# Optimization experiments

Hardware: AMD Instinct MI355X
Metric: run time of the kernel (lower is better)

## Reference

```python
import jax, jax.numpy as jnp
import numpy as np

B, V, C_IN, C_OUT = 4, 8, 32, 32
H, W = 256, 256
G = H * W
K_NEIGHBORS = 3


def compute_adjacency_tilde(extrinsics, k):
    Bv, Vv = extrinsics.shape[:2]
    R = extrinsics[:, :, :3, :3]
    t = extrinsics[:, :, :3, 3]
    # camera centers: -R^T t
    centers = -jnp.einsum('bvji,bvj->bvi', R, t)                 # (B,V,3)
    diff = centers[:, :, None, :] - centers[:, None, :, :]
    dist_sq = jnp.sum(diff * diff, axis=-1)                      # (B,V,V)
    eye = jnp.eye(Vv, dtype=bool)
    sim = jnp.where(eye, -jnp.inf, -dist_sq)
    A_overlap = 1.0 / (1.0 + jnp.sqrt(dist_sq + 1e-6))
    if 0 < k < Vv:
        _, topk_idx = jax.lax.top_k(sim, k)                      # (B,V,k)
        mask = jnp.sum(jax.nn.one_hot(topk_idx, Vv, dtype=jnp.float32), axis=-2) > 0
        A = A_overlap * mask.astype(A_overlap.dtype)
    else:
        A = A_overlap
    A = jnp.where(eye, 1.0, A)                                   # diagonal = 1
    deg = jnp.sum(A, axis=-1, keepdims=True)
    A_tilde = A / (deg + (deg == 0).astype(deg.dtype))
    return A, A_tilde


def setup_inputs() -> dict:
    key = jax.random.key(0)
    k1, k2, k3, k4, k5 = jax.random.split(key, 5)
    features = jax.random.normal(k1, (B, V, G, C_IN), dtype=jnp.float32)
    # projected pixel coords in [0, W-1] x [0, H-1]
    uv = jax.random.uniform(k2, (B, V, V, G, 2), dtype=jnp.float32)
    xy_coords = uv * jnp.array([W - 1, H - 1], dtype=jnp.float32)
    extrinsics = jax.random.normal(k3, (B, V, 4, 4), dtype=jnp.float32)
    W_lin = jax.random.normal(k4, (C_IN, C_OUT), dtype=jnp.float32) * 0.1
    b_lin = jax.random.normal(k5, (C_OUT,), dtype=jnp.float32) * 0.01
    return {"features": features, "xy_coords": xy_coords, "extrinsics": extrinsics,
            "W_lin": W_lin, "b_lin": b_lin}


def reference(features, xy_coords, extrinsics, W_lin, b_lin):
    feats = features @ W_lin + b_lin                              # (B,V,G,D)
    Bv, Vv, Gv, D = feats.shape
    HW = H * W
    A, A_tilde = compute_adjacency_tilde(extrinsics, K_NEIGHBORS)
    # flattened pixel indices per (batch, src view, tgt view, gaussian)
    x = jnp.clip(jnp.round(xy_coords[..., 0]), 0, W - 1).astype(jnp.int32)
    y = jnp.clip(jnp.round(xy_coords[..., 1]), 0, H - 1).astype(jnp.int32)
    idx = y * W + x                                               # (B,Vsrc,Vtgt,G)
    batch_off = jnp.arange(Bv, dtype=jnp.int32)[:, None] * HW
    outs = []
    for i in range(Vv):  # small fixed number of target views
        w_i = A_tilde[:, i][:, :, None, None]                     # (B,Vsrc,1,1)
        data = (feats * w_i).reshape(Bv * Vv * Gv, D)
        seg = (idx[:, :, i].reshape(Bv, Vv * Gv) + batch_off).reshape(-1)
        grid = jax.ops.segment_sum(data, seg, num_segments=Bv * HW)
        grid = grid.reshape(Bv, HW, D)                            # (B,HW,D)
        self_idx = idx[:, i, i]                                   # (B,G)
        outs.append(jnp.take_along_axis(grid, self_idx[..., None], axis=1))
    stacked = jnp.stack(outs, axis=1)                             # (B,V,G,D)
    return stacked, A
```

## Files before the change

### kernel.cpp

```cpp
#include <hip/hip_runtime.h>
#include <math.h>

#define NB 4
#define NV 8
#define NC 32
#define NG 65536
#define IMGW 256
#define NBI 32
#define RSPLIT 8
#define RBINS (NG / RSPLIT)
#define K4SPLIT 32
#define K4BINS (NG / K4SPLIT)
#define K4CAP 24576
#define CAP4A 1272
#define PART_STRIDE 19456
#define START_STRIDE 65544
#define SORT_STRIDE (1u << 20)
#define SENTINEL (8u << 27)

static constexpr long long STACKED_ELEMS = (long long)NB * NV * NG * NC;

typedef __attribute__((ext_vector_type(8))) short short8;
typedef __attribute__((ext_vector_type(4))) float f32x4;
typedef __attribute__((ext_vector_type(4))) unsigned int u32x4;
typedef __attribute__((ext_vector_type(4))) float f32x4c;

static constexpr size_t OFF_AT    = 0;
static constexpr size_t OFF_RTOT  = 1024;
static constexpr size_t OFF_RBASE = 2048;
static constexpr size_t OFF_GSC   = 3584;
static constexpr size_t OFF_START = 8192;
static constexpr size_t OFF_CNT   = OFF_START + (size_t)NBI * START_STRIDE * 4;
static constexpr size_t OFF_PIX   = OFF_CNT + (size_t)NBI * NG * 4;
static constexpr size_t OFF_SORT  = OFF_PIX + (size_t)NBI * NV * NG * 2;
static constexpr size_t OFF_FB16  = OFF_SORT + (size_t)NBI * SORT_STRIDE * 4;
static constexpr size_t OFF_PARTS = OFF_FB16;

__device__ __forceinline__ unsigned short f2bf(float f)
{
    unsigned int u = __float_as_uint(f);
    return (unsigned short)((u + 0x7FFFu + ((u >> 16) & 1u)) >> 16);
}

__global__ __launch_bounds__(256) void adj_kernel(const float* __restrict__ ext,
                                                  float* __restrict__ A_out,
                                                  float* __restrict__ At_out)
{
    __shared__ float ctr[NB * NV][3];
    __shared__ float Dsh[NB * NV * NV];
    int t = threadIdx.x;
    if (t < NB * NV) {
        const float* E = ext + t * 16;
        #pragma unroll
        for (int i = 0; i < 3; i++) {
            float s = E[0 * 4 + i] * E[0 * 4 + 3]
                    + E[1 * 4 + i] * E[1 * 4 + 3]
                    + E[2 * 4 + i] * E[2 * 4 + 3];
            ctr[t][i] = -s;
        }
    }
    __syncthreads();
    {
        int b = t >> 6, i = (t >> 3) & 7, j = t & 7;
        float dx = ctr[b * 8 + i][0] - ctr[b * 8 + j][0];
        float dy = ctr[b * 8 + i][1] - ctr[b * 8 + j][1];
        float dz = ctr[b * 8 + i][2] - ctr[b * 8 + j][2];
        Dsh[t] = dx * dx + dy * dy + dz * dz;
    }
    __syncthreads();
    if (t < NB * NV) {
        int ri = t & 7;
        const float* drow = &Dsh[t * 8];
        bool chosen[8] = {false, false, false, false, false, false, false, false};
        for (int n = 0; n < 3; n++) {
            int best = -1; float bs = -3.0e38f;
            for (int j2 = 0; j2 < 8; j2++) {
                if (j2 == ri || chosen[j2]) continue;
                float s = -drow[j2];
                if (s > bs) { bs = s; best = j2; }
            }
            chosen[best] = true;
        }
        float row[8]; float deg = 0.f;
        #pragma unroll
        for (int j2 = 0; j2 < 8; j2++) {
            float a = 0.f;
            if (j2 == ri)        a = 1.0f;
            else if (chosen[j2]) a = 1.0f / (1.0f + sqrtf(drow[j2] + 1e-6f));
            row[j2] = a; deg += a;
        }
        float dn = deg + (deg == 0.f ? 1.f : 0.f);
        #pragma unroll
        for (int j2 = 0; j2 < 8; j2++) {
            A_out[t * 8 + j2]  = row[j2];
            At_out[t * 8 + j2] = row[j2] / dn;
        }
    }
}

__global__ __launch_bounds__(256) void k1_pix(const float2* __restrict__ xy,
                                              unsigned short* __restrict__ pixarr)
{
    unsigned int base = blockIdx.x * 1024 + threadIdx.x;
    #pragma unroll
    for (int k = 0; k < 4; k++) {
        unsigned int tid = base + k * 256;
        float2 p = xy[tid];
        float px = fminf(fmaxf(rintf(p.x), 0.f), (float)(IMGW - 1));
        float py = fminf(fmaxf(rintf(p.y), 0.f), (float)(IMGW - 1));
        unsigned int pix = (unsigned int)py * IMGW + (unsigned int)px;
        unsigned int g = tid & 0xFFFFu;
        unsigned int i = (tid >> 16) & 7u;
        unsigned int j = (tid >> 19) & 7u;
        unsigned int b = tid >> 22;
        unsigned int bi = (b << 3) | i;
        pixarr[(((bi << 3) | j) << 16) | g] = (unsigned short)pix;
    }
}

__global__ __launch_bounds__(1024) void k2_hist(const unsigned short* __restrict__ pixarr,
                                                unsigned int* __restrict__ cnt,
                                                unsigned int* __restrict__ rtot)
{
    __shared__ unsigned int hist[RBINS];
    int t = threadIdx.x;
    unsigned int bi = blockIdx.x & 31u;
    unsigned int r  = blockIdx.x >> 5;
    unsigned int r0 = r * RBINS;
    for (int k = t; k < RBINS; k += 1024) hist[k] = 0;
    __syncthreads();
    const uint4* src = (const uint4*)(pixarr + ((size_t)bi << 19));
    for (int it = 0; it < 16; it++) {
        uint4 vv[4];
        #pragma unroll
        for (int q = 0; q < 4; q++)
            vv[q] = src[t + (it * 4 + q) * 1024];
        #pragma unroll
        for (int q = 0; q < 4; q++) {
            const unsigned int* vw = (const unsigned int*)&vv[q];
            #pragma unroll
            for (int h = 0; h < 4; h++) {
                unsigned int w = vw[h];
                unsigned int p0 = (w & 0xFFFFu) - r0;
                unsigned int p1 = (w >> 16) - r0;
                if (p0 < RBINS) atomicAdd(&hist[p0], 1u);
                if (p1 < RBINS) atomicAdd(&hist[p1], 1u);
            }
        }
    }
    __syncthreads();
    unsigned int* dst = cnt + ((size_t)bi << 16) + r0;
    unsigned int psum = 0;
    for (int k = t; k < RBINS; k += 1024) {
        unsigned int v = hist[k];
        dst[k] = v;
        psum += (v + 7u) & ~7u;
    }
    __syncthreads();
    hist[t] = psum;
    __syncthreads();
    for (int off = 512; off; off >>= 1) {
        if (t < off) hist[t] += hist[t + off];
        __syncthreads();
    }
    if (t == 0) rtot[bi * 8 + r] = hist[0];
}

__global__ __launch_bounds__(64) void k3b_rscan(const unsigned int* __restrict__ rtot,
                                                unsigned int* __restrict__ rbase)
{
    int t = threadIdx.x;
    if (t < 32) {
        unsigned int run = 0;
        #pragma unroll
        for (int q = 0; q < 8; q++) {
            rbase[t * 9 + q] = run;
            run += rtot[t * 8 + q];
        }
        rbase[t * 9 + 8] = run;
    }
}

__global__ __launch_bounds__(1024) void k3c_scan(const unsigned int* __restrict__ cnt,
                                                 const unsigned int* __restrict__ rbase,
                                                 unsigned int* __restrict__ start)
{
    __shared__ unsigned int lc[RBINS];
    __shared__ unsigned int bs[1024];
    int t = threadIdx.x;
    unsigned int bi = blockIdx.x & 31u;
    unsigned int r  = blockIdx.x >> 5;
    unsigned int r0 = r * RBINS;
    const unsigned int* c = cnt + ((size_t)bi << 16) + r0;
    #pragma unroll
    for (int q = 0; q < 8; q++)
        lc[q * 1024 + t] = (c[q * 1024 + t] + 7u) & ~7u;
    __syncthreads();
    unsigned int v[8]; unsigned int s = 0;
    #pragma unroll
    for (int k = 0; k < 8; k++) { v[k] = s; s += lc[t * 8 + k]; }
    bs[t] = s;
    __syncthreads();
    for (int off = 1; off < 1024; off <<= 1) {
        unsigned int u = (t >= off) ? bs[t - off] : 0u;
        __syncthreads();
        bs[t] += u;
        __syncthreads();
    }
    unsigned int base = rbase[bi * 9 + r] + bs[t] - s;
    #pragma unroll
    for (int k = 0; k < 8; k++) lc[t * 8 + k] = base + v[k];
    __syncthreads();
    unsigned int* st_ = start + (size_t)bi * START_STRIDE + r0;
    #pragma unroll
    for (int q = 0; q < 8; q++)
        st_[q * 1024 + t] = lc[q * 1024 + t];
    if (r == 7 && t == 0)
        start[(size_t)bi * START_STRIDE + NG] = rbase[bi * 9 + 8];
}

__global__ __launch_bounds__(1024) void k4a_part(const unsigned short* __restrict__ pixarr,
                                                 unsigned int* __restrict__ gsc,
                                                 unsigned int* __restrict__ parts)
{
    extern __shared__ unsigned int dynA[];
    unsigned int* cur32 = dynA;
    unsigned int* res   = dynA + 32;
    unsigned int* lcnt  = dynA + 64;
    unsigned int* lbuck = dynA + 96;
    int t = threadIdx.x;
    unsigned int bi    = blockIdx.x & 31u;
    unsigned int chunk = blockIdx.x >> 5;
    if (t < 32) cur32[t] = 0;
    __syncthreads();
    const uint4* src = (const uint4*)(pixarr + ((size_t)bi << 19)) + (chunk << 12);
    unsigned int idx0 = chunk << 15;
    #pragma unroll
    for (int it = 0; it < 4; it++) {
        uint4 v = src[t + it * 1024];
        unsigned int base_idx = idx0 + (t + it * 1024) * 8;
        const unsigned int* vw = (const unsigned int*)&v;
        #pragma unroll
        for (int h = 0; h < 8; h++) {
            unsigned int pix = (h & 1) ? (vw[h >> 1] >> 16) : (vw[h >> 1] & 0xFFFFu);
            unsigned int sub = pix >> 11;
            unsigned int pv = ((pix & 0x7FFu) << 19) | (base_idx + h);
            unsigned int slot = atomicAdd(&cur32[sub], 1u);
            if (slot < CAP4A) {
                lbuck[sub * CAP4A + slot] = pv;
            } else {
                unsigned int gs = atomicAdd(&gsc[(bi << 5) | sub], 1u);
                parts[(size_t)((bi << 5) | sub) * PART_STRIDE + gs] = pv;
            }
        }
    }
    __syncthreads();
    if (t < 32) {
        unsigned int n = cur32[t];
        n = n < CAP4A ? n : CAP4A;
        lcnt[t] = n;
        res[t] = atomicAdd(&gsc[(bi << 5) | t], n);
    }
    __syncthreads();
    for (int s = 0; s < 32; s++) {
        unsigned int n = lcnt[s];
        unsigned int b0 = res[s];
        unsigned int* dst = parts + (size_t)((bi << 5) | s) * PART_STRIDE + b0;
        const unsigned int* sb = lbuck + s * CAP4A;
        for (unsigned int k = t; k < n; k += 1024) dst[k] = sb[k];
    }
}

__global__ __launch_bounds__(1024) void k4b_fill(const unsigned int* __restrict__ gsc,
                                                 const unsigned int* __restrict__ parts,
                                                 const unsigned int* __restrict__ start,
                                                 unsigned int* __restrict__ sorted)
{
    extern __shared__ unsigned int dynB[];
    unsigned int* cur = dynB;
    unsigned int* buf = dynB + K4BINS;
    int t = threadIdx.x;
    unsigned int bi  = blockIdx.x & 31u;
    unsigned int sub = blockIdx.x >> 5;
    unsigned int bin0 = sub * K4BINS;
    const unsigned int* stg = start + (size_t)bi * START_STRIDE;
    unsigned int base = stg[bin0];
    unsigned int end  = stg[bin0 + K4BINS];
    unsigned int size = end - base;
    unsigned int n = gsc[(bi << 5) | sub];
    const unsigned int* seg = parts + (size_t)((bi << 5) | sub) * PART_STRIDE;
    unsigned int* dstbase = sorted + (size_t)bi * SORT_STRIDE;

    if (size <= K4CAP) {
        #pragma unroll 2
        for (int k = t; k < K4BINS; k += 1024) cur[k] = stg[bin0 + k] - base;
        for (int k = t; k < (int)size; k += 1024) buf[k] = SENTINEL;
        __syncthreads();
        for (unsigned int k = t; k < n; k += 1024) {
            unsigned int pv = seg[k];
            unsigned int bin = pv >> 19;
            unsigned int slot = atomicAdd(&cur[bin], 1u);
            buf[slot] = (((pv >> 16) & 7u) << 27) | ((pv & 0x7FFFFu) << 6);
        }
        __syncthreads();
        uint4* gdst = (uint4*)(dstbase + base);
        const uint4* lsrc = (const uint4*)buf;
        int n4 = (int)(size >> 2);
        for (int k = t; k < n4; k += 1024) gdst[k] = lsrc[k];
    } else {
        #pragma unroll 2
        for (int k = t; k < K4BINS; k += 1024) cur[k] = stg[bin0 + k];
        __syncthreads();
        for (unsigned int k = t; k < n; k += 1024) {
            unsigned int pv = seg[k];
            unsigned int bin = pv >> 19;
            unsigned int slot = atomicAdd(&cur[bin], 1u);
            dstbase[slot] = (((pv >> 16) & 7u) << 27) | ((pv & 0x7FFFFu) << 6);
        }
        __syncthreads();
        for (int k = t; k < K4BINS; k += 1024) {
            unsigned int e = stg[bin0 + k + 1];
            for (unsigned int x = cur[k]; x < e; x++) dstbase[x] = SENTINEL;
        }
    }
}

__global__ __launch_bounds__(256) void kf_conv(const float* __restrict__ src,
                                               ushort4* __restrict__ dst)
{
    unsigned int base = blockIdx.x * 1024 + threadIdx.x;
    #pragma unroll
    for (int k = 0; k < 4; k++) {
        unsigned int idx = base + k * 256;
        f32x4c v = __builtin_nontemporal_load((const f32x4c*)(src) + idx);
        ushort4 o;
        o.x = f2bf(v.x); o.y = f2bf(v.y); o.z = f2bf(v.z); o.w = f2bf(v.w);
        dst[idx] = o;
    }
}

__global__ __launch_bounds__(256, 4) void b_gather(
    const unsigned short* __restrict__ fb16,
    const unsigned short* __restrict__ pixarr,
    const unsigned int* __restrict__ start,
    const unsigned int* __restrict__ sorted,
    const float* __restrict__ Wlin,
    const float* __restrict__ blin,
    const float* __restrict__ At,
    float* __restrict__ out,
    int b)
{
    __shared__ float At9[NBI][16];
    int t = threadIdx.x;
    int c4 = t & 7;
    int grp = t >> 3;

    unsigned int bidx = blockIdx.x;
    unsigned int i  = bidx & 7u;
    unsigned int gc = bidx >> 3;
    unsigned int bi = ((unsigned int)b << 3) | i;
    unsigned int g0 = gc << 5;
    unsigned int g = g0 + grp;
    unsigned int pix = pixarr[(((bi << 3) | i) << 16) | g];

    At9[t >> 3][t & 7] = At[t];
    At9[t >> 3][8 + (t & 7)] = 0.f;

    int l = t & 63;
    short8 bf0, bf1;
    #pragma unroll
    for (int j = 0; j < 8; j++) {
        int kk = (l >> 4) * 8 + j;
        bf0[j] = (short)f2bf(Wlin[kk * NC + (l & 15)]);
        bf1[j] = (short)f2bf(Wlin[kk * NC + 16 + (l & 15)]);
    }

    const unsigned int* st = start + (size_t)bi * START_STRIDE;
    unsigned int s0 = st[pix];
    unsigned int e0 = st[pix + 1];
    const unsigned int* pl = sorted + (size_t)bi * SORT_STRIDE;
    const char* fbB = (const char*)fb16;
    unsigned int cb = c4 << 3;
    __syncthreads();

    const float* Atrow = At9[bi];
    float ax = 0.f, ay = 0.f, az = 0.f, aw = 0.f, wsum = 0.f;
    for (unsigned int k0 = s0; k0 < e0; k0 += 8) {
        u32x4 pa = __builtin_nontemporal_load((const u32x4*)(pl + k0));
        u32x4 pb = __builtin_nontemporal_load((const u32x4*)(pl + k0 + 4));
        unsigned int pv[8] = {pa.x, pa.y, pa.z, pa.w, pb.x, pb.y, pb.z, pb.w};
        uint2 uv[8];
        #pragma unroll
        for (int h = 0; h < 8; h++)
            uv[h] = *(const uint2*)(fbB + ((pv[h] & 0x01FFFFC0u) | cb));
        float wv[8];
        #pragma unroll
        for (int h = 0; h < 8; h++)
            wv[h] = Atrow[pv[h] >> 27];
        #pragma unroll
        for (int h = 0; h < 8; h++) {
            ax = fmaf(wv[h], __uint_as_float(uv[h].x << 16), ax);
            ay = fmaf(wv[h], __uint_as_float(uv[h].x & 0xFFFF0000u), ay);
            az = fmaf(wv[h], __uint_as_float(uv[h].y << 16), az);
            aw = fmaf(wv[h], __uint_as_float(uv[h].y & 0xFFFF0000u), aw);
            wsum += wv[h];
        }
    }

    int r = l & 15;
    int kb = l >> 4;
    int s0l = (((r & 7) << 3) | (kb << 1)) & 63;
    int s1l = s0l | 1;
    float v0x = __shfl(ax, s0l, 64), v0y = __shfl(ay, s0l, 64);
    float v0z = __shfl(az, s0l, 64), v0w = __shfl(aw, s0l, 64);
    float v1x = __shfl(ax, s1l, 64), v1y = __shfl(ay, s1l, 64);
    float v1z = __shfl(az, s1l, 64), v1w = __shfl(aw, s1l, 64);
    short8 af;
    if (r < 8) {
        af[0] = (short)f2bf(v0x); af[1] = (short)f2bf(v0y);
        af[2] = (short)f2bf(v0z); af[3] = (short)f2bf(v0w);
        af[4] = (short)f2bf(v1x); af[5] = (short)f2bf(v1y);
        af[6] = (short)f2bf(v1z); af[7] = (short)f2bf(v1w);
    } else {
        af = short8{0, 0, 0, 0, 0, 0, 0, 0};
    }
    float bias0 = blin[l & 15];
    float bias1 = blin[16 + (l & 15)];
    f32x4 c0, c1;
    #pragma unroll
    for (int q = 0; q < 4; q++) {
        int row = kb * 4 + q;
        float wvx = __shfl(wsum, (row << 3) & 63, 64);
        wvx = (row < 8) ? wvx : 0.f;
        c0[q] = bias0 * wvx;
        c1[q] = bias1 * wvx;
    }
    c0 = __builtin_amdgcn_mfma_f32_16x16x32_bf16(af, bf0, c0, 0, 0, 0);
    c1 = __builtin_amdgcn_mfma_f32_16x16x32_bf16(af, bf1, c1, 0, 0, 0);
    if (l < 32) {
        size_t rowbase = (((size_t)bi << 16) | g0) + (t >> 6) * 8;
        #pragma unroll
        for (int q = 0; q < 4; q++) {
            size_t rr = rowbase + (l >> 4) * 4 + q;
            __builtin_nontemporal_store(c0[q], &out[rr * NC + (l & 15)]);
            __builtin_nontemporal_store(c1[q], &out[rr * NC + 16 + (l & 15)]);
        }
    }
}

extern "C" void kernel_launch(void* const* d_in, const int* in_sizes, int n_in,
                              void* d_out, int out_size, void* d_ws, size_t ws_size,
                              hipStream_t stream)
{
    const float* features = (const float*)d_in[0];
    const float* xy       = (const float*)d_in[1];
    const float* ext      = (const float*)d_in[2];
    const float* Wlin     = (const float*)d_in[3];
    const float* blin     = (const float*)d_in[4];
    float* out = (float*)d_out;

    char* ws = (char*)d_ws;
    float*          At     = (float*)(ws + OFF_AT);
    unsigned int*   rtot   = (unsigned int*)(ws + OFF_RTOT);
    unsigned int*   rbase  = (unsigned int*)(ws + OFF_RBASE);
    unsigned int*   gsc    = (unsigned int*)(ws + OFF_GSC);
    unsigned int*   start  = (unsigned int*)(ws + OFF_START);
    unsigned int*   cnt    = (unsigned int*)(ws + OFF_CNT);
    unsigned short* pixarr = (unsigned short*)(ws + OFF_PIX);
    unsigned int*   sorted = (unsigned int*)(ws + OFF_SORT);
    unsigned int*   parts  = (unsigned int*)(ws + OFF_PARTS);
    unsigned short* fb16   = (unsigned short*)(ws + OFF_FB16);

    static const size_t k4a_lds = (96 + 32 * CAP4A) * sizeof(unsigned int);
    static const size_t k4b_lds = (K4BINS + K4CAP) * sizeof(unsigned int);
    hipFuncSetAttribute((const void*)k4a_part,
                        hipFuncAttributeMaxDynamicSharedMemorySize, (int)k4a_lds);
    hipFuncSetAttribute((const void*)k4b_fill,
                        hipFuncAttributeMaxDynamicSharedMemorySize, (int)k4b_lds);

    adj_kernel<<<1, 256, 0, stream>>>(ext, out + STACKED_ELEMS, At);

    k1_pix<<<(NB * NV * NV * NG) / 1024, 256, 0, stream>>>((const float2*)xy, pixarr);
    k2_hist<<<NBI * RSPLIT, 1024, 0, stream>>>(pixarr, cnt, rtot);
    k3b_rscan<<<1, 64, 0, stream>>>(rtot, rbase);
    k3c_scan<<<NBI * RSPLIT, 1024, 0, stream>>>(cnt, rbase, start);

    hipMemsetAsync(gsc, 0, 1024 * sizeof(unsigned int), stream);
    k4a_part<<<NBI * 16, 1024, k4a_lds, stream>>>(pixarr, gsc, parts);
    k4b_fill<<<NBI * K4SPLIT, 1024, k4b_lds, stream>>>(gsc, parts, start, sorted);

    for (int b = 0; b < NB; b++) {
        const float* src = features + (((size_t)b) << 19) * NC;
        kf_conv<<<4096, 256, 0, stream>>>(src, (ushort4*)fb16);
        b_gather<<<16384, 256, 0, stream>>>(fb16, pixarr, start, sorted,
                                            Wlin, blin, At, out, b);
    }
}
```

Before: 599.1 us.

## Fold adjacency and row-scan kernels into neighbours, prefetch gather indices

The adjacency computation becomes an extra block of the pixel-index kernel, and the tiny row-scan kernel is removed: each scan block now sums the per-range totals itself. This cuts two kernel launches and their serialisation gaps. The histogram loop now loads 8 vectors per iteration instead of 4 to put more memory requests in flight. The gather kernel issues its first sorted-index loads before the setup work and software-pipelines the next index loads under the feature loads, which costs extra registers.

```diff
diff --git a/kernel.cpp b/kernel.cpp
--- a/kernel.cpp
+++ b/kernel.cpp
@@ -27,7 +27,6 @@
 
 static constexpr size_t OFF_AT    = 0;
 static constexpr size_t OFF_RTOT  = 1024;
-static constexpr size_t OFF_RBASE = 2048;
 static constexpr size_t OFF_GSC   = 3584;
 static constexpr size_t OFF_START = 8192;
 static constexpr size_t OFF_CNT   = OFF_START + (size_t)NBI * START_STRIDE * 4;
@@ -42,65 +41,65 @@
     return (unsigned short)((u + 0x7FFFu + ((u >> 16) & 1u)) >> 16);
 }
 
-__global__ __launch_bounds__(256) void adj_kernel(const float* __restrict__ ext,
-                                                  float* __restrict__ A_out,
-                                                  float* __restrict__ At_out)
-{
-    __shared__ float ctr[NB * NV][3];
-    __shared__ float Dsh[NB * NV * NV];
-    int t = threadIdx.x;
-    if (t < NB * NV) {
-        const float* E = ext + t * 16;
-        #pragma unroll
-        for (int i = 0; i < 3; i++) {
-            float s = E[0 * 4 + i] * E[0 * 4 + 3]
-                    + E[1 * 4 + i] * E[1 * 4 + 3]
-                    + E[2 * 4 + i] * E[2 * 4 + 3];
-            ctr[t][i] = -s;
-        }
-    }
-    __syncthreads();
-    {
-        int b = t >> 6, i = (t >> 3) & 7, j = t & 7;
-        float dx = ctr[b * 8 + i][0] - ctr[b * 8 + j][0];
-        float dy = ctr[b * 8 + i][1] - ctr[b * 8 + j][1];
-        float dz = ctr[b * 8 + i][2] - ctr[b * 8 + j][2];
-        Dsh[t] = dx * dx + dy * dy + dz * dz;
-    }
-    __syncthreads();
-    if (t < NB * NV) {
-        int ri = t & 7;
-        const float* drow = &Dsh[t * 8];
-        bool chosen[8] = {false, false, false, false, false, false, false, false};
-        for (int n = 0; n < 3; n++) {
-            int best = -1; float bs = -3.0e38f;
+__global__ __launch_bounds__(256) void k1_pix(const float2* __restrict__ xy,
+                                              unsigned short* __restrict__ pixarr,
+                                              const float* __restrict__ ext,
+                                              float* __restrict__ A_out,
+                                              float* __restrict__ At_out)
+{
+    if (blockIdx.x == 16384) {
+        __shared__ float ctr[NB * NV][3];
+        __shared__ float Dsh[NB * NV * NV];
+        int t = threadIdx.x;
+        if (t < NB * NV) {
+            const float* E = ext + t * 16;
+            #pragma unroll
+            for (int i = 0; i < 3; i++) {
+                float s = E[0 * 4 + i] * E[0 * 4 + 3]
+                        + E[1 * 4 + i] * E[1 * 4 + 3]
+                        + E[2 * 4 + i] * E[2 * 4 + 3];
+                ctr[t][i] = -s;
+            }
+        }
+        __syncthreads();
+        {
+            int b = t >> 6, i = (t >> 3) & 7, j = t & 7;
+            float dx = ctr[b * 8 + i][0] - ctr[b * 8 + j][0];
+            float dy = ctr[b * 8 + i][1] - ctr[b * 8 + j][1];
+            float dz = ctr[b * 8 + i][2] - ctr[b * 8 + j][2];
+            Dsh[t] = dx * dx + dy * dy + dz * dz;
+        }
+        __syncthreads();
+        if (t < NB * NV) {
+            int ri = t & 7;
+            const float* drow = &Dsh[t * 8];
+            bool chosen[8] = {false, false, false, false, false, false, false, false};
+            for (int n = 0; n < 3; n++) {
+                int best = -1; float bs = -3.0e38f;
+                for (int j2 = 0; j2 < 8; j2++) {
+                    if (j2 == ri || chosen[j2]) continue;
+                    float s = -drow[j2];
+                    if (s > bs) { bs = s; best = j2; }
+                }
+                chosen[best] = true;
+            }
+            float row[8]; float deg = 0.f;
+            #pragma unroll
             for (int j2 = 0; j2 < 8; j2++) {
-                if (j2 == ri || chosen[j2]) continue;
-                float s = -drow[j2];
-                if (s > bs) { bs = s; best = j2; }
-            }
-            chosen[best] = true;
-        }
-        float row[8]; float deg = 0.f;
-        #pragma unroll
-        for (int j2 = 0; j2 < 8; j2++) {
-            float a = 0.f;
-            if (j2 == ri)        a = 1.0f;
-            else if (chosen[j2]) a = 1.0f / (1.0f + sqrtf(drow[j2] + 1e-6f));
-            row[j2] = a; deg += a;
-        }
-        float dn = deg + (deg == 0.f ? 1.f : 0.f);
-        #pragma unroll
-        for (int j2 = 0; j2 < 8; j2++) {
-            A_out[t * 8 + j2]  = row[j2];
-            At_out[t * 8 + j2] = row[j2] / dn;
-        }
-    }
-}
-
-__global__ __launch_bounds__(256) void k1_pix(const float2* __restrict__ xy,
-                                              unsigned short* __restrict__ pixarr)
-{
+                float a = 0.f;
+                if (j2 == ri)        a = 1.0f;
+                else if (chosen[j2]) a = 1.0f / (1.0f + sqrtf(drow[j2] + 1e-6f));
+                row[j2] = a; deg += a;
+            }
+            float dn = deg + (deg == 0.f ? 1.f : 0.f);
+            #pragma unroll
+            for (int j2 = 0; j2 < 8; j2++) {
+                A_out[t * 8 + j2]  = row[j2];
+                At_out[t * 8 + j2] = row[j2] / dn;
+            }
+        }
+        return;
+    }
     unsigned int base = blockIdx.x * 1024 + threadIdx.x;
     #pragma unroll
     for (int k = 0; k < 4; k++) {
@@ -130,13 +129,13 @@
     for (int k = t; k < RBINS; k += 1024) hist[k] = 0;
     __syncthreads();
     const uint4* src = (const uint4*)(pixarr + ((size_t)bi << 19));
-    for (int it = 0; it < 16; it++) {
-        uint4 vv[4];
-        #pragma unroll
-        for (int q = 0; q < 4; q++)
-            vv[q] = src[t + (it * 4 + q) * 1024];
-        #pragma unroll
-        for (int q = 0; q < 4; q++) {
+    for (int it = 0; it < 8; it++) {
+        uint4 vv[8];
+        #pragma unroll
+        for (int q = 0; q < 8; q++)
+            vv[q] = src[t + (it * 8 + q) * 1024];
+        #pragma unroll
+        for (int q = 0; q < 8; q++) {
             const unsigned int* vw = (const unsigned int*)&vv[q];
             #pragma unroll
             for (int h = 0; h < 4; h++) {
@@ -166,23 +165,8 @@
     if (t == 0) rtot[bi * 8 + r] = hist[0];
 }
 
-__global__ __launch_bounds__(64) void k3b_rscan(const unsigned int* __restrict__ rtot,
-                                                unsigned int* __restrict__ rbase)
-{
-    int t = threadIdx.x;
-    if (t < 32) {
-        unsigned int run = 0;
-        #pragma unroll
-        for (int q = 0; q < 8; q++) {
-            rbase[t * 9 + q] = run;
-            run += rtot[t * 8 + q];
-        }
-        rbase[t * 9 + 8] = run;
-    }
-}
-
 __global__ __launch_bounds__(1024) void k3c_scan(const unsigned int* __restrict__ cnt,
-                                                 const unsigned int* __restrict__ rbase,
+                                                 const unsigned int* __restrict__ rtot,
                                                  unsigned int* __restrict__ start)
 {
     __shared__ unsigned int lc[RBINS];
@@ -191,6 +175,13 @@
     unsigned int bi = blockIdx.x & 31u;
     unsigned int r  = blockIdx.x >> 5;
     unsigned int r0 = r * RBINS;
+    unsigned int rb = 0, rtotal = 0;
+    #pragma unroll
+    for (int q = 0; q < 8; q++) {
+        unsigned int v = rtot[bi * 8 + q];
+        if ((unsigned int)q < r) rb += v;
+        rtotal += v;
+    }
     const unsigned int* c = cnt + ((size_t)bi << 16) + r0;
     #pragma unroll
     for (int q = 0; q < 8; q++)
@@ -207,7 +198,7 @@
         bs[t] += u;
         __syncthreads();
     }
-    unsigned int base = rbase[bi * 9 + r] + bs[t] - s;
+    unsigned int base = rb + bs[t] - s;
     #pragma unroll
     for (int k = 0; k < 8; k++) lc[t * 8 + k] = base + v[k];
     __syncthreads();
@@ -216,7 +207,7 @@
     for (int q = 0; q < 8; q++)
         st_[q * 1024 + t] = lc[q * 1024 + t];
     if (r == 7 && t == 0)
-        start[(size_t)bi * START_STRIDE + NG] = rbase[bi * 9 + 8];
+        start[(size_t)bi * START_STRIDE + NG] = rtotal;
 }
 
 __global__ __launch_bounds__(1024) void k4a_part(const unsigned short* __restrict__ pixarr,
@@ -361,11 +352,17 @@
     unsigned int bi = ((unsigned int)b << 3) | i;
     unsigned int g0 = gc << 5;
     unsigned int g = g0 + grp;
+
     unsigned int pix = pixarr[(((bi << 3) | i) << 16) | g];
+    const unsigned int* st = start + (size_t)bi * START_STRIDE;
+    unsigned int s0 = st[pix];
+    unsigned int e0 = st[pix + 1];
+    const unsigned int* pl = sorted + (size_t)bi * SORT_STRIDE;
+    u32x4 pa = __builtin_nontemporal_load((const u32x4*)(pl + s0));
+    u32x4 pb = __builtin_nontemporal_load((const u32x4*)(pl + s0 + 4));
 
     At9[t >> 3][t & 7] = At[t];
     At9[t >> 3][8 + (t & 7)] = 0.f;
-
     int l = t & 63;
     short8 bf0, bf1;
     #pragma unroll
@@ -374,11 +371,6 @@
         bf0[j] = (short)f2bf(Wlin[kk * NC + (l & 15)]);
         bf1[j] = (short)f2bf(Wlin[kk * NC + 16 + (l & 15)]);
     }
-
-    const unsigned int* st = start + (size_t)bi * START_STRIDE;
-    unsigned int s0 = st[pix];
-    unsigned int e0 = st[pix + 1];
-    const unsigned int* pl = sorted + (size_t)bi * SORT_STRIDE;
     const char* fbB = (const char*)fb16;
     unsigned int cb = c4 << 3;
     __syncthreads();
@@ -386,13 +378,15 @@
     const float* Atrow = At9[bi];
     float ax = 0.f, ay = 0.f, az = 0.f, aw = 0.f, wsum = 0.f;
     for (unsigned int k0 = s0; k0 < e0; k0 += 8) {
-        u32x4 pa = __builtin_nontemporal_load((const u32x4*)(pl + k0));
-        u32x4 pb = __builtin_nontemporal_load((const u32x4*)(pl + k0 + 4));
         unsigned int pv[8] = {pa.x, pa.y, pa.z, pa.w, pb.x, pb.y, pb.z, pb.w};
         uint2 uv[8];
         #pragma unroll
         for (int h = 0; h < 8; h++)
             uv[h] = *(const uint2*)(fbB + ((pv[h] & 0x01FFFFC0u) | cb));
+        if (k0 + 8 < e0) {
+            pa = __builtin_nontemporal_load((const u32x4*)(pl + k0 + 8));
+            pb = __builtin_nontemporal_load((const u32x4*)(pl + k0 + 12));
+        }
         float wv[8];
         #pragma unroll
         for (int h = 0; h < 8; h++)
@@ -462,7 +456,6 @@
     char* ws = (char*)d_ws;
     float*          At     = (float*)(ws + OFF_AT);
     unsigned int*   rtot   = (unsigned int*)(ws + OFF_RTOT);
-    unsigned int*   rbase  = (unsigned int*)(ws + OFF_RBASE);
     unsigned int*   gsc    = (unsigned int*)(ws + OFF_GSC);
     unsigned int*   start  = (unsigned int*)(ws + OFF_START);
     unsigned int*   cnt    = (unsigned int*)(ws + OFF_CNT);
@@ -478,12 +471,10 @@
     hipFuncSetAttribute((const void*)k4b_fill,
                         hipFuncAttributeMaxDynamicSharedMemorySize, (int)k4b_lds);
 
-    adj_kernel<<<1, 256, 0, stream>>>(ext, out + STACKED_ELEMS, At);
-
-    k1_pix<<<(NB * NV * NV * NG) / 1024, 256, 0, stream>>>((const float2*)xy, pixarr);
+    k1_pix<<<16385, 256, 0, stream>>>((const float2*)xy, pixarr, ext,
+                                      out + STACKED_ELEMS, At);
     k2_hist<<<NBI * RSPLIT, 1024, 0, stream>>>(pixarr, cnt, rtot);
-    k3b_rscan<<<1, 64, 0, stream>>>(rtot, rbase);
-    k3c_scan<<<NBI * RSPLIT, 1024, 0, stream>>>(cnt, rbase, start);
+    k3c_scan<<<NBI * RSPLIT, 1024, 0, stream>>>(cnt, rtot, start);
 
     hipMemsetAsync(gsc, 0, 1024 * sizeof(unsigned int), stream);
     k4a_part<<<NBI * 16, 1024, k4a_lds, stream>>>(pixarr, gsc, parts);
```

New measurement: 592.1 us. No clear change (-1.2%).
